# Optimization experiments

Hardware: AMD Instinct MI355X
Metric: run time of the kernel (lower is better)

Reference implementation:

```python
import jax, jax.numpy as jnp
import numpy as np

N_NODES = 100000
N_EDGES = 1600000
N_GRAPHS = 64
D_NODE = 32
D_EDGE = 32
D_U = 32
OUT_DIM = 64
IN1 = 2 * D_NODE + D_EDGE + D_U  # 128
IN2 = D_NODE + OUT_DIM + D_U      # 128


def setup_inputs() -> dict:
    key = jax.random.key(0)
    ks = jax.random.split(key, 9)
    x = jax.random.normal(ks[0], (N_NODES, D_NODE), dtype=jnp.float32)
    edge_index = jax.random.randint(ks[1], (2, N_EDGES), 0, N_NODES, dtype=jnp.int64)
    edge_attr = jax.random.normal(ks[2], (N_EDGES, D_EDGE), dtype=jnp.float32)
    u = jax.random.normal(ks[3], (N_GRAPHS, D_U), dtype=jnp.float32)
    batch = jnp.sort(jax.random.randint(ks[4], (N_NODES,), 0, N_GRAPHS, dtype=jnp.int64))
    W1 = jax.random.normal(ks[5], (IN1, OUT_DIM), dtype=jnp.float32) * (1.0 / np.sqrt(IN1))
    b1 = jax.random.normal(ks[6], (OUT_DIM,), dtype=jnp.float32) * 0.01
    W2 = jax.random.normal(ks[7], (IN2, OUT_DIM), dtype=jnp.float32) * (1.0 / np.sqrt(IN2))
    b2 = jax.random.normal(ks[8], (OUT_DIM,), dtype=jnp.float32) * 0.01
    return {"x": x, "edge_index": edge_index, "edge_attr": edge_attr, "u": u,
            "batch": batch, "W1": W1, "b1": b1, "W2": W2, "b2": b2}


def reference(x, edge_index, edge_attr, u, batch, W1, b1, W2, b2):
    src, dest = edge_index[0], edge_index[1]
    u_node = u[batch]                     # [N_NODES, D_U]
    u_edge = u_node[src]                  # [N_EDGES, D_U] == u[batch][src]
    # Edge-level MLP1: concat gathered features then Linear+ReLU
    m_in = jnp.concatenate([x[dest], x[src], edge_attr, u_edge], axis=-1)
    messages = jax.nn.relu(m_in @ W1 + b1)            # [N_EDGES, OUT_DIM]
    # scatter-sum messages onto destination nodes
    agg = jax.ops.segment_sum(messages, dest, num_segments=x.shape[0])
    # Node-level MLP2
    n_in = jnp.concatenate([x, agg, u_node], axis=-1)  # [N_NODES, IN2]
    return jax.nn.relu(n_in @ W2 + b2)                 # [N_NODES, OUT_DIM]
```

## Files before the change

### kernel.cpp

```cpp
#include <hip/hip_runtime.h>


constexpr int kNodes  = 100000;
constexpr int kEdges  = 1600000;
constexpr int kGraphs = 64;
constexpr int kD      = 32;
constexpr int kOut    = 64;
constexpr int kTiles  = kEdges / 16;
constexpr int SB      = 256;
constexpr int NB      = (kNodes + SB - 1) / SB;
static_assert(kEdges % 16 == 0, "tile-exact");
static_assert(NB <= 512, "scan_top handles <=512 block sums");

using frag_b = __attribute__((ext_vector_type(8))) short;
using f32x4  = __attribute__((ext_vector_type(4))) float;

__device__ __forceinline__ short f2bf(float f) {
  unsigned u = __float_as_uint(f);
  return (short)((u + 0x7FFFu + ((u >> 16) & 1u)) >> 16);
}
__device__ __forceinline__ unsigned pk2bf(float lo, float hi) {
  return (unsigned)(unsigned short)f2bf(lo) |
         ((unsigned)(unsigned short)f2bf(hi) << 16);
}
__device__ __forceinline__ float bf2f(short h) {
  return __uint_as_float((unsigned)(unsigned short)h << 16);
}
__device__ __forceinline__ float bflo(unsigned w) {
  return __uint_as_float(w << 16);
}
__device__ __forceinline__ float bfhi(unsigned w) {
  return __uint_as_float(w & 0xFFFF0000u);
}

__global__ __launch_bounds__(256) void cvt_kernel(const float* __restrict__ src,
                                                  short* __restrict__ dst,
                                                  int n4) {
  int i = blockIdx.x * 256 + threadIdx.x;
  int stride = gridDim.x * 256;
  for (; i < n4; i += stride) {
    float4 v = reinterpret_cast<const float4*>(src)[i];
    short4 h;
    h.x = f2bf(v.x); h.y = f2bf(v.y); h.z = f2bf(v.z); h.w = f2bf(v.w);
    reinterpret_cast<short4*>(dst)[i] = h;
  }
}

__global__ __launch_bounds__(256) void w1pack_kernel(
    const float* __restrict__ W1, uint4* __restrict__ W1p) {
  int idx = blockIdx.x * 256 + threadIdx.x;
  if (idx >= 1024) return;
  int lane = idx & 63, ntile = (idx >> 6) & 3, ts = idx >> 8;
  int n  = ntile * 16 + (lane & 15);
  int k0 = ts * 32 + ((lane >> 4) & 3) * 8;
  unsigned w[4];
#pragma unroll
  for (int p = 0; p < 4; ++p)
    w[p] = pk2bf(W1[(size_t)(k0 + 2 * p) * kOut + n],
                 W1[(size_t)(k0 + 2 * p + 1) * kOut + n]);
  W1p[idx] = make_uint4(w[0], w[1], w[2], w[3]);
}

__global__ __launch_bounds__(256) void tables_kernel(
    const float* __restrict__ u, const float* __restrict__ W2,
    const float* __restrict__ b2, float* __restrict__ U2) {
  int t = blockIdx.x * 256 + threadIdx.x;
  if (t >= kGraphs * kOut) return;
  int g = t >> 6, j = t & 63;
  float a2 = b2[j];
#pragma unroll
  for (int k = 0; k < kD; ++k)
    a2 = fmaf(u[g * kD + k], W2[(size_t)(96 + k) * kOut + j], a2);
  U2[t] = a2;
}

__global__ __launch_bounds__(256) void hist_kernel(const int* __restrict__ ei,
                                                   int* __restrict__ counts) {
  int i = blockIdx.x * 256 + threadIdx.x;
  int stride = gridDim.x * 256;
  for (int e = i; e < kEdges; e += stride)
    atomicAdd(&counts[ei[kEdges + e]], 1);
}

__global__ __launch_bounds__(SB) void scan_reduce(const int* __restrict__ counts,
                                                  int* __restrict__ bsum) {
  __shared__ int s[SB];
  int i = blockIdx.x * SB + threadIdx.x;
  s[threadIdx.x] = (i < kNodes) ? counts[i] : 0;
  __syncthreads();
  for (int off = SB / 2; off > 0; off >>= 1) {
    if (threadIdx.x < off) s[threadIdx.x] += s[threadIdx.x + off];
    __syncthreads();
  }
  if (threadIdx.x == 0) bsum[blockIdx.x] = s[0];
}

__global__ __launch_bounds__(512) void scan_top(int* __restrict__ bsum) {
  __shared__ int s[512];
  int t = threadIdx.x;
  int orig = (t < NB) ? bsum[t] : 0;
  s[t] = orig;
  __syncthreads();
  for (int off = 1; off < 512; off <<= 1) {
    int a = (t >= off) ? s[t - off] : 0;
    __syncthreads();
    s[t] += a;
    __syncthreads();
  }
  if (t < NB) bsum[t] = s[t] - orig;
}

__global__ __launch_bounds__(SB) void scan_final(
    const int* __restrict__ counts, const int* __restrict__ bscan,
    int* __restrict__ offs, int* __restrict__ cursor) {
  __shared__ int s[SB];
  int i = blockIdx.x * SB + threadIdx.x;
  int v = (i < kNodes) ? counts[i] : 0;
  s[threadIdx.x] = v;
  __syncthreads();
  for (int off = 1; off < SB; off <<= 1) {
    int a = (threadIdx.x >= off) ? s[threadIdx.x - off] : 0;
    __syncthreads();
    s[threadIdx.x] += a;
    __syncthreads();
  }
  if (i < kNodes) {
    int ex = s[threadIdx.x] - v + bscan[blockIdx.x];
    offs[i] = ex;
    cursor[i] = ex;
  }
  if (blockIdx.x == 0 && threadIdx.x == 0) offs[kNodes] = kEdges;
}

__global__ __launch_bounds__(256) void slot_kernel(const int* __restrict__ ei,
                                                   int* __restrict__ cursor,
                                                   int* __restrict__ pos) {
  int i = blockIdx.x * 256 + threadIdx.x;
  int stride = gridDim.x * 256;
  for (int e = i; e < kEdges; e += stride)
    pos[e] = atomicAdd(&cursor[ei[kEdges + e]], 1);
}

__global__ __launch_bounds__(256) void edge_mfma_kernel(
    const int* __restrict__ ei, const int* __restrict__ batch,
    const short* __restrict__ xb, const float* __restrict__ ea,
    const short* __restrict__ ub, const uint4* __restrict__ W1p,
    const float* __restrict__ b1, const int* __restrict__ pos,
    short* __restrict__ msgbuf) {
  __shared__ uint4 sW[1024];
  for (int i = threadIdx.x; i < 1024; i += 256) sW[i] = W1p[i];
  __syncthreads();
  const int lane = threadIdx.x & 63;
  const int er   = lane & 15;
  const int kq   = lane >> 4;
  const int koff = kq * 8;
  float b1v[4];
#pragma unroll
  for (int n = 0; n < 4; ++n) b1v[n] = b1[n * 16 + er];
  const int wave = (blockIdx.x * 256 + threadIdx.x) >> 6;
  const int nw   = gridDim.x * 4;
  for (int t = wave; t < kTiles; t += nw) {
    const int tb = t * 16;
    const int s  = ei[tb + er];
    const int d  = ei[kEdges + tb + er];
    const int g  = batch[s];
    const uint4 pv = *reinterpret_cast<const uint4*>(pos + tb + kq * 4);
    frag_b a0 = *reinterpret_cast<const frag_b*>(xb + (size_t)d * kD + koff);
    frag_b a1 = *reinterpret_cast<const frag_b*>(xb + (size_t)s * kD + koff);
    const float4* ef =
        reinterpret_cast<const float4*>(ea + (size_t)(tb + er) * kD + koff);
    float4 e0 = ef[0], e1 = ef[1];
    frag_b a3 = *reinterpret_cast<const frag_b*>(ub + g * kD + koff);
    union { frag_b f; unsigned w[4]; } a2u;
    a2u.w[0] = pk2bf(e0.x, e0.y);
    a2u.w[1] = pk2bf(e0.z, e0.w);
    a2u.w[2] = pk2bf(e1.x, e1.y);
    a2u.w[3] = pk2bf(e1.z, e1.w);
    f32x4 acc[4];
#pragma unroll
    for (int n = 0; n < 4; ++n) {
      acc[n] = (f32x4){0.f, 0.f, 0.f, 0.f};
      acc[n] = __builtin_amdgcn_mfma_f32_16x16x32_bf16(
          a0, *reinterpret_cast<const frag_b*>(&sW[(0 * 4 + n) * 64 + lane]),
          acc[n], 0, 0, 0);
      acc[n] = __builtin_amdgcn_mfma_f32_16x16x32_bf16(
          a1, *reinterpret_cast<const frag_b*>(&sW[(1 * 4 + n) * 64 + lane]),
          acc[n], 0, 0, 0);
      acc[n] = __builtin_amdgcn_mfma_f32_16x16x32_bf16(
          a2u.f, *reinterpret_cast<const frag_b*>(&sW[(2 * 4 + n) * 64 + lane]),
          acc[n], 0, 0, 0);
      acc[n] = __builtin_amdgcn_mfma_f32_16x16x32_bf16(
          a3, *reinterpret_cast<const frag_b*>(&sW[(3 * 4 + n) * 64 + lane]),
          acc[n], 0, 0, 0);
    }
    const int prow[4] = {(int)pv.x, (int)pv.y, (int)pv.z, (int)pv.w};
#pragma unroll
    for (int n = 0; n < 4; ++n)
#pragma unroll
      for (int r = 0; r < 4; ++r) {
        float v = fmaxf(acc[n][r] + b1v[n], 0.f);
        msgbuf[(size_t)prow[r] * kOut + n * 16 + er] = f2bf(v);
      }
  }
}

__global__ __launch_bounds__(256) void sum_mlp2_kernel(
    const float* __restrict__ x, const short* __restrict__ msgbuf,
    const int* __restrict__ offs, const int* __restrict__ batch,
    const float* __restrict__ U2, const float* __restrict__ W2,
    float* __restrict__ out) {
  __shared__ float sWa[kD * kOut];
  __shared__ float sWb[kOut * kOut];
  __shared__ float aggrow[4 * kOut];
  for (int i = threadIdx.x; i < kD * kOut; i += 256) sWa[i] = W2[i];
  for (int i = threadIdx.x; i < kOut * kOut; i += 256)
    sWb[i] = W2[kD * kOut + i];
  __syncthreads();
  const int lane = threadIdx.x & 63;
  const int wv   = threadIdx.x >> 6;
  const int wave = (blockIdx.x * 256 + threadIdx.x) >> 6;
  const int nw   = gridDim.x * 4;
  const int c0   = (lane & 7) * 8;
  for (int n = wave; n < kNodes; n += nw) {
    const int rb = offs[n], re = offs[n + 1];
    float vs[8];
#pragma unroll
    for (int j = 0; j < 8; ++j) vs[j] = 0.f;
    int r = rb;
    for (; r + 8 <= re; r += 8) {
      uint4 w = reinterpret_cast<const uint4*>(msgbuf + (size_t)r * kOut)[lane];
      vs[0] += bflo(w.x); vs[1] += bfhi(w.x);
      vs[2] += bflo(w.y); vs[3] += bfhi(w.y);
      vs[4] += bflo(w.z); vs[5] += bfhi(w.z);
      vs[6] += bflo(w.w); vs[7] += bfhi(w.w);
    }
#pragma unroll
    for (int st = 8; st < 64; st <<= 1)
#pragma unroll
      for (int j = 0; j < 8; ++j) vs[j] += __shfl_xor(vs[j], st);
#pragma unroll
    for (int j = 0; j < 8; ++j) aggrow[wv * kOut + c0 + j] = vs[j];
    float tail = 0.f;
    for (; r < re; ++r) tail += bf2f(msgbuf[(size_t)r * kOut + lane]);
    aggrow[wv * kOut + lane] += tail;
    float acc = U2[batch[n] * kOut + lane];
    const float4* xr = reinterpret_cast<const float4*>(x + (size_t)n * kD);
#pragma unroll
    for (int q = 0; q < 8; ++q) {
      float4 v = xr[q];
      int k = q * 4;
      acc = fmaf(v.x, sWa[(k + 0) * kOut + lane], acc);
      acc = fmaf(v.y, sWa[(k + 1) * kOut + lane], acc);
      acc = fmaf(v.z, sWa[(k + 2) * kOut + lane], acc);
      acc = fmaf(v.w, sWa[(k + 3) * kOut + lane], acc);
    }
#pragma unroll
    for (int q = 0; q < 16; ++q) {
      float4 v = *reinterpret_cast<const float4*>(&aggrow[wv * kOut + q * 4]);
      int k = q * 4;
      acc = fmaf(v.x, sWb[(k + 0) * kOut + lane], acc);
      acc = fmaf(v.y, sWb[(k + 1) * kOut + lane], acc);
      acc = fmaf(v.z, sWb[(k + 2) * kOut + lane], acc);
      acc = fmaf(v.w, sWb[(k + 3) * kOut + lane], acc);
    }
    out[(size_t)n * kOut + lane] = fmaxf(acc, 0.f);
  }
}

extern "C" void kernel_launch(void* const* d_in, const int* in_sizes, int n_in,
                              void* d_out, int out_size, void* d_ws,
                              size_t ws_size, hipStream_t stream) {
  const float* x     = (const float*)d_in[0];
  const int*   ei    = (const int*)d_in[1];
  const float* ea    = (const float*)d_in[2];
  const float* u     = (const float*)d_in[3];
  const int*   batch = (const int*)d_in[4];
  const float* W1    = (const float*)d_in[5];
  const float* b1    = (const float*)d_in[6];
  const float* W2    = (const float*)d_in[7];
  const float* b2    = (const float*)d_in[8];
  float* out = (float*)d_out;

  auto align256 = [](char* p) {
    return (char*)(((size_t)p + 255) & ~(size_t)255);
  };
  char* p = (char*)d_ws;
  uint4* W1p = (uint4*)p;                 p = align256(p + 1024 * 16);
  float* U2  = (float*)p;                 p = align256(p + kGraphs * kOut * 4);
  int* counts = (int*)p;                  p = align256(p + kNodes * 4);
  int* offs   = (int*)p;                  p = align256(p + (kNodes + 1) * 4);
  int* cursor = (int*)p;                  p = align256(p + kNodes * 4);
  int* bsum   = (int*)p;                  p = align256(p + 512 * 4);
  int* pos    = (int*)p;                  p = align256(p + (size_t)kEdges * 4);
  short* xb   = (short*)p;                p = align256(p + (size_t)kNodes * kD * 2);
  short* ub   = (short*)p;                p = align256(p + kGraphs * kD * 2);
  short* msgbuf = (short*)p;

  hipMemsetAsync(counts, 0, (size_t)kNodes * sizeof(int), stream);
  cvt_kernel<<<512, 256, 0, stream>>>(x, xb, kNodes * kD / 4);
  cvt_kernel<<<2, 256, 0, stream>>>(u, ub, kGraphs * kD / 4);
  w1pack_kernel<<<4, 256, 0, stream>>>(W1, W1p);
  tables_kernel<<<(kGraphs * kOut + 255) / 256, 256, 0, stream>>>(u, W2, b2,
                                                                  U2);
  hist_kernel<<<2048, 256, 0, stream>>>(ei, counts);
  scan_reduce<<<NB, SB, 0, stream>>>(counts, bsum);
  scan_top<<<1, 512, 0, stream>>>(bsum);
  scan_final<<<NB, SB, 0, stream>>>(counts, bsum, offs, cursor);
  slot_kernel<<<2048, 256, 0, stream>>>(ei, cursor, pos);
  edge_mfma_kernel<<<2048, 256, 0, stream>>>(ei, batch, xb, ea, ub, W1p, b1,
                                             pos, msgbuf);
  sum_mlp2_kernel<<<2048, 256, 0, stream>>>(x, msgbuf, offs, batch, U2, W2,
                                            out);
}
```

Before: 767.4 us.

## Sort edges by destination and fuse message compute with shared-memory segment sum

The slot kernel now writes a packed per-edge record (edge id, local dest, src, graph) into destination-sorted order. A new edge kernel walks each 64-node block's contiguous edge range, computes messages with MFMA and reduces them into shared-memory accumulators via run-length segmented adds before writing fp32 agg. This removes the bf16 message buffer round trip (write plus reread). In exchange, edge_attr is now gathered in random order and LDS atomics are added. The small setup kernels are merged into one prep launch.

```diff
diff --git a/kernel.cpp b/kernel.cpp
--- a/kernel.cpp
+++ b/kernel.cpp
@@ -6,9 +6,10 @@
 constexpr int kGraphs = 64;
 constexpr int kD      = 32;
 constexpr int kOut    = 64;
-constexpr int kTiles  = kEdges / 16;
 constexpr int SB      = 256;
 constexpr int NB      = (kNodes + SB - 1) / SB;
+constexpr int NPB     = 64;
+constexpr int NAB     = (kNodes + NPB - 1) / NPB;
 static_assert(kEdges % 16 == 0, "tile-exact");
 static_assert(NB <= 512, "scan_top handles <=512 block sums");
 
@@ -23,55 +24,52 @@
   return (unsigned)(unsigned short)f2bf(lo) |
          ((unsigned)(unsigned short)f2bf(hi) << 16);
 }
-__device__ __forceinline__ float bf2f(short h) {
-  return __uint_as_float((unsigned)(unsigned short)h << 16);
-}
-__device__ __forceinline__ float bflo(unsigned w) {
-  return __uint_as_float(w << 16);
-}
-__device__ __forceinline__ float bfhi(unsigned w) {
-  return __uint_as_float(w & 0xFFFF0000u);
-}
-
-__global__ __launch_bounds__(256) void cvt_kernel(const float* __restrict__ src,
-                                                  short* __restrict__ dst,
-                                                  int n4) {
-  int i = blockIdx.x * 256 + threadIdx.x;
-  int stride = gridDim.x * 256;
-  for (; i < n4; i += stride) {
-    float4 v = reinterpret_cast<const float4*>(src)[i];
-    short4 h;
-    h.x = f2bf(v.x); h.y = f2bf(v.y); h.z = f2bf(v.z); h.w = f2bf(v.w);
-    reinterpret_cast<short4*>(dst)[i] = h;
-  }
-}
-
-__global__ __launch_bounds__(256) void w1pack_kernel(
-    const float* __restrict__ W1, uint4* __restrict__ W1p) {
-  int idx = blockIdx.x * 256 + threadIdx.x;
-  if (idx >= 1024) return;
-  int lane = idx & 63, ntile = (idx >> 6) & 3, ts = idx >> 8;
-  int n  = ntile * 16 + (lane & 15);
-  int k0 = ts * 32 + ((lane >> 4) & 3) * 8;
-  unsigned w[4];
-#pragma unroll
-  for (int p = 0; p < 4; ++p)
-    w[p] = pk2bf(W1[(size_t)(k0 + 2 * p) * kOut + n],
-                 W1[(size_t)(k0 + 2 * p + 1) * kOut + n]);
-  W1p[idx] = make_uint4(w[0], w[1], w[2], w[3]);
-}
-
-__global__ __launch_bounds__(256) void tables_kernel(
-    const float* __restrict__ u, const float* __restrict__ W2,
-    const float* __restrict__ b2, float* __restrict__ U2) {
-  int t = blockIdx.x * 256 + threadIdx.x;
-  if (t >= kGraphs * kOut) return;
-  int g = t >> 6, j = t & 63;
-  float a2 = b2[j];
-#pragma unroll
-  for (int k = 0; k < kD; ++k)
-    a2 = fmaf(u[g * kD + k], W2[(size_t)(96 + k) * kOut + j], a2);
-  U2[t] = a2;
+
+__global__ __launch_bounds__(256) void prep_kernel(
+    const float* __restrict__ x, const float* __restrict__ u,
+    const float* __restrict__ W1, const float* __restrict__ W2,
+    const float* __restrict__ b2, short* __restrict__ xb,
+    short* __restrict__ ub, uint4* __restrict__ W1p, float* __restrict__ U2) {
+  const int bid = blockIdx.x, tid = threadIdx.x;
+  if (bid < 512) {
+    const int n4 = kNodes * kD / 4;
+    for (int i = bid * 256 + tid; i < n4; i += 512 * 256) {
+      float4 v = reinterpret_cast<const float4*>(x)[i];
+      short4 h;
+      h.x = f2bf(v.x); h.y = f2bf(v.y); h.z = f2bf(v.z); h.w = f2bf(v.w);
+      reinterpret_cast<short4*>(xb)[i] = h;
+    }
+  } else if (bid == 512) {
+    for (int i = tid; i < kGraphs * kD / 4; i += 256) {
+      float4 v = reinterpret_cast<const float4*>(u)[i];
+      short4 h;
+      h.x = f2bf(v.x); h.y = f2bf(v.y); h.z = f2bf(v.z); h.w = f2bf(v.w);
+      reinterpret_cast<short4*>(ub)[i] = h;
+    }
+  } else if (bid < 517) {
+    int idx = (bid - 513) * 256 + tid;
+    if (idx < 1024) {
+      int lane = idx & 63, ntile = (idx >> 6) & 3, ts = idx >> 8;
+      int n  = ntile * 16 + (lane & 15);
+      int k0 = ts * 32 + ((lane >> 4) & 3) * 8;
+      unsigned w[4];
+#pragma unroll
+      for (int p = 0; p < 4; ++p)
+        w[p] = pk2bf(W1[(size_t)(k0 + 2 * p) * kOut + n],
+                     W1[(size_t)(k0 + 2 * p + 1) * kOut + n]);
+      W1p[idx] = make_uint4(w[0], w[1], w[2], w[3]);
+    }
+  } else {
+    int t = (bid - 517) * 256 + tid;
+    if (t < kGraphs * kOut) {
+      int g = t >> 6, j = t & 63;
+      float a2 = b2[j];
+#pragma unroll
+      for (int k = 0; k < kD; ++k)
+        a2 = fmaf(u[g * kD + k], W2[(size_t)(96 + k) * kOut + j], a2);
+      U2[t] = a2;
+    }
+  }
 }
 
 __global__ __launch_bounds__(256) void hist_kernel(const int* __restrict__ ei,
@@ -132,43 +130,56 @@
   if (blockIdx.x == 0 && threadIdx.x == 0) offs[kNodes] = kEdges;
 }
 
-__global__ __launch_bounds__(256) void slot_kernel(const int* __restrict__ ei,
-                                                   int* __restrict__ cursor,
-                                                   int* __restrict__ pos) {
+__global__ __launch_bounds__(256) void slot_kernel(
+    const int* __restrict__ ei, const int* __restrict__ batch,
+    int* __restrict__ cursor, uint2* __restrict__ urec) {
   int i = blockIdx.x * 256 + threadIdx.x;
   int stride = gridDim.x * 256;
-  for (int e = i; e < kEdges; e += stride)
-    pos[e] = atomicAdd(&cursor[ei[kEdges + e]], 1);
-}
-
-__global__ __launch_bounds__(256) void edge_mfma_kernel(
-    const int* __restrict__ ei, const int* __restrict__ batch,
+  for (int e = i; e < kEdges; e += stride) {
+    int s = ei[e];
+    int d = ei[kEdges + e];
+    int g = batch[s];
+    int p = atomicAdd(&cursor[d], 1);
+    urec[p] = make_uint2((unsigned)e | ((unsigned)(d & 63) << 21),
+                         (unsigned)s | ((unsigned)g << 17));
+  }
+}
+
+__global__ __launch_bounds__(256) void edge_agg_kernel(
+    const uint2* __restrict__ urec, const int* __restrict__ offs,
     const short* __restrict__ xb, const float* __restrict__ ea,
     const short* __restrict__ ub, const uint4* __restrict__ W1p,
-    const float* __restrict__ b1, const int* __restrict__ pos,
-    short* __restrict__ msgbuf) {
+    const float* __restrict__ b1, float* __restrict__ agg) {
   __shared__ uint4 sW[1024];
-  for (int i = threadIdx.x; i < 1024; i += 256) sW[i] = W1p[i];
-  __syncthreads();
-  const int lane = threadIdx.x & 63;
+  __shared__ float sAcc[NPB * kOut];
+  __shared__ float msgT[4][16 * 64];
+  const int tid  = threadIdx.x;
+  const int lane = tid & 63;
+  const int wv   = tid >> 6;
   const int er   = lane & 15;
   const int kq   = lane >> 4;
   const int koff = kq * 8;
+  for (int i = tid; i < 1024; i += 256) sW[i] = W1p[i];
+  for (int i = tid; i < NPB * kOut; i += 256) sAcc[i] = 0.f;
+  __syncthreads();
   float b1v[4];
 #pragma unroll
   for (int n = 0; n < 4; ++n) b1v[n] = b1[n * 16 + er];
-  const int wave = (blockIdx.x * 256 + threadIdx.x) >> 6;
-  const int nw   = gridDim.x * 4;
-  for (int t = wave; t < kTiles; t += nw) {
-    const int tb = t * 16;
-    const int s  = ei[tb + er];
-    const int d  = ei[kEdges + tb + er];
-    const int g  = batch[s];
-    const uint4 pv = *reinterpret_cast<const uint4*>(pos + tb + kq * 4);
+  const int n0  = blockIdx.x * NPB;
+  const int n1  = min(n0 + NPB, kNodes);
+  const int beg = offs[n0], end = offs[n1];
+  const int tb0 = (beg >> 4) << 4;
+  for (int tb = tb0 + (wv << 4); tb < end; tb += 64) {
+    const uint2 rc = urec[tb + er];
+    const int e  = min((int)(rc.x & 0x1FFFFFu), kEdges - 1);
+    const int dl = (int)((rc.x >> 21) & 63u);
+    const int s  = min((int)(rc.y & 0x1FFFFu), kNodes - 1);
+    const int g  = (int)(rc.y >> 17) & 63;
+    const int d  = min(n0 + dl, kNodes - 1);
     frag_b a0 = *reinterpret_cast<const frag_b*>(xb + (size_t)d * kD + koff);
     frag_b a1 = *reinterpret_cast<const frag_b*>(xb + (size_t)s * kD + koff);
     const float4* ef =
-        reinterpret_cast<const float4*>(ea + (size_t)(tb + er) * kD + koff);
+        reinterpret_cast<const float4*>(ea + (size_t)e * kD + koff);
     float4 e0 = ef[0], e1 = ef[1];
     frag_b a3 = *reinterpret_cast<const frag_b*>(ub + g * kD + koff);
     union { frag_b f; unsigned w[4]; } a2u;
@@ -193,56 +204,52 @@
           a3, *reinterpret_cast<const frag_b*>(&sW[(3 * 4 + n) * 64 + lane]),
           acc[n], 0, 0, 0);
     }
-    const int prow[4] = {(int)pv.x, (int)pv.y, (int)pv.z, (int)pv.w};
-#pragma unroll
-    for (int n = 0; n < 4; ++n)
+#pragma unroll
+    for (int n = 0; n < 4; ++n) {
+      const int c = n * 16 + er;
 #pragma unroll
       for (int r = 0; r < 4; ++r) {
-        float v = fmaxf(acc[n][r] + b1v[n], 0.f);
-        msgbuf[(size_t)prow[r] * kOut + n * 16 + er] = f2bf(v);
+        const int row = kq * 4 + r;
+        msgT[wv][row * 64 + ((c + row * 8) & 63)] =
+            fmaxf(acc[n][r] + b1v[n], 0.f);
       }
-  }
-}
-
-__global__ __launch_bounds__(256) void sum_mlp2_kernel(
-    const float* __restrict__ x, const short* __restrict__ msgbuf,
-    const int* __restrict__ offs, const int* __restrict__ batch,
-    const float* __restrict__ U2, const float* __restrict__ W2,
-    float* __restrict__ out) {
+    }
+    float al = 0.f;
+    int dcur = -1;
+#pragma unroll
+    for (int r = 0; r < 16; ++r) {
+      const int q = tb + r;
+      if (q < beg || q >= end) continue;
+      const int dr = __shfl(dl, r);
+      const float v = msgT[wv][r * 64 + ((lane + r * 8) & 63)];
+      if (dr != dcur) {
+        if (dcur >= 0) unsafeAtomicAdd(&sAcc[dcur * kOut + lane], al);
+        al = 0.f;
+        dcur = dr;
+      }
+      al += v;
+    }
+    if (dcur >= 0) unsafeAtomicAdd(&sAcc[dcur * kOut + lane], al);
+  }
+  __syncthreads();
+  for (int r = wv; r < n1 - n0; r += 4)
+    agg[(size_t)(n0 + r) * kOut + lane] = sAcc[r * kOut + lane];
+}
+
+__global__ __launch_bounds__(256) void mlp2_kernel(
+    const float* __restrict__ x, const float* __restrict__ agg,
+    const int* __restrict__ batch, const float* __restrict__ U2,
+    const float* __restrict__ W2, float* __restrict__ out) {
   __shared__ float sWa[kD * kOut];
   __shared__ float sWb[kOut * kOut];
-  __shared__ float aggrow[4 * kOut];
   for (int i = threadIdx.x; i < kD * kOut; i += 256) sWa[i] = W2[i];
   for (int i = threadIdx.x; i < kOut * kOut; i += 256)
     sWb[i] = W2[kD * kOut + i];
   __syncthreads();
   const int lane = threadIdx.x & 63;
-  const int wv   = threadIdx.x >> 6;
   const int wave = (blockIdx.x * 256 + threadIdx.x) >> 6;
   const int nw   = gridDim.x * 4;
-  const int c0   = (lane & 7) * 8;
   for (int n = wave; n < kNodes; n += nw) {
-    const int rb = offs[n], re = offs[n + 1];
-    float vs[8];
-#pragma unroll
-    for (int j = 0; j < 8; ++j) vs[j] = 0.f;
-    int r = rb;
-    for (; r + 8 <= re; r += 8) {
-      uint4 w = reinterpret_cast<const uint4*>(msgbuf + (size_t)r * kOut)[lane];
-      vs[0] += bflo(w.x); vs[1] += bfhi(w.x);
-      vs[2] += bflo(w.y); vs[3] += bfhi(w.y);
-      vs[4] += bflo(w.z); vs[5] += bfhi(w.z);
-      vs[6] += bflo(w.w); vs[7] += bfhi(w.w);
-    }
-#pragma unroll
-    for (int st = 8; st < 64; st <<= 1)
-#pragma unroll
-      for (int j = 0; j < 8; ++j) vs[j] += __shfl_xor(vs[j], st);
-#pragma unroll
-    for (int j = 0; j < 8; ++j) aggrow[wv * kOut + c0 + j] = vs[j];
-    float tail = 0.f;
-    for (; r < re; ++r) tail += bf2f(msgbuf[(size_t)r * kOut + lane]);
-    aggrow[wv * kOut + lane] += tail;
     float acc = U2[batch[n] * kOut + lane];
     const float4* xr = reinterpret_cast<const float4*>(x + (size_t)n * kD);
 #pragma unroll
@@ -254,9 +261,10 @@
       acc = fmaf(v.z, sWa[(k + 2) * kOut + lane], acc);
       acc = fmaf(v.w, sWa[(k + 3) * kOut + lane], acc);
     }
+    const float4* ar = reinterpret_cast<const float4*>(agg + (size_t)n * kOut);
 #pragma unroll
     for (int q = 0; q < 16; ++q) {
-      float4 v = *reinterpret_cast<const float4*>(&aggrow[wv * kOut + q * 4]);
+      float4 v = ar[q];
       int k = q * 4;
       acc = fmaf(v.x, sWb[(k + 0) * kOut + lane], acc);
       acc = fmaf(v.y, sWb[(k + 1) * kOut + lane], acc);
@@ -285,30 +293,25 @@
     return (char*)(((size_t)p + 255) & ~(size_t)255);
   };
   char* p = (char*)d_ws;
-  uint4* W1p = (uint4*)p;                 p = align256(p + 1024 * 16);
-  float* U2  = (float*)p;                 p = align256(p + kGraphs * kOut * 4);
-  int* counts = (int*)p;                  p = align256(p + kNodes * 4);
-  int* offs   = (int*)p;                  p = align256(p + (kNodes + 1) * 4);
-  int* cursor = (int*)p;                  p = align256(p + kNodes * 4);
-  int* bsum   = (int*)p;                  p = align256(p + 512 * 4);
-  int* pos    = (int*)p;                  p = align256(p + (size_t)kEdges * 4);
-  short* xb   = (short*)p;                p = align256(p + (size_t)kNodes * kD * 2);
-  short* ub   = (short*)p;                p = align256(p + kGraphs * kD * 2);
-  short* msgbuf = (short*)p;
+  uint4* W1p  = (uint4*)p;  p = align256(p + 1024 * 16);
+  float* U2   = (float*)p;  p = align256(p + kGraphs * kOut * 4);
+  int* counts = (int*)p;    p = align256(p + kNodes * 4);
+  int* offs   = (int*)p;    p = align256(p + (kNodes + 1) * 4);
+  int* cursor = (int*)p;    p = align256(p + kNodes * 4);
+  int* bsum   = (int*)p;    p = align256(p + 512 * 4);
+  short* xb   = (short*)p;  p = align256(p + (size_t)kNodes * kD * 2);
+  short* ub   = (short*)p;  p = align256(p + kGraphs * kD * 2);
+  uint2* urec = (uint2*)p;  p = align256(p + (size_t)(kEdges + 16) * 8);
+  float* agg  = (float*)p;
 
   hipMemsetAsync(counts, 0, (size_t)kNodes * sizeof(int), stream);
-  cvt_kernel<<<512, 256, 0, stream>>>(x, xb, kNodes * kD / 4);
-  cvt_kernel<<<2, 256, 0, stream>>>(u, ub, kGraphs * kD / 4);
-  w1pack_kernel<<<4, 256, 0, stream>>>(W1, W1p);
-  tables_kernel<<<(kGraphs * kOut + 255) / 256, 256, 0, stream>>>(u, W2, b2,
-                                                                  U2);
+  prep_kernel<<<533, 256, 0, stream>>>(x, u, W1, W2, b2, xb, ub, W1p, U2);
   hist_kernel<<<2048, 256, 0, stream>>>(ei, counts);
   scan_reduce<<<NB, SB, 0, stream>>>(counts, bsum);
   scan_top<<<1, 512, 0, stream>>>(bsum);
   scan_final<<<NB, SB, 0, stream>>>(counts, bsum, offs, cursor);
-  slot_kernel<<<2048, 256, 0, stream>>>(ei, cursor, pos);
-  edge_mfma_kernel<<<2048, 256, 0, stream>>>(ei, batch, xb, ea, ub, W1p, b1,
-                                             pos, msgbuf);
-  sum_mlp2_kernel<<<2048, 256, 0, stream>>>(x, msgbuf, offs, batch, U2, W2,
-                                            out);
-}
+  slot_kernel<<<2048, 256, 0, stream>>>(ei, batch, cursor, urec);
+  edge_agg_kernel<<<NAB, 256, 0, stream>>>(urec, offs, xb, ea, ub, W1p, b1,
+                                           agg);
+  mlp2_kernel<<<2048, 256, 0, stream>>>(x, agg, batch, U2, W2, out);
+}
```

Result: faster. 747.9 us (-2.5%).
